# Optimization experiments

Measured on AMD Instinct MI355X. Metric: run time of the kernel, lower is better.

The kernel has to match this reference:

```python
import jax, jax.numpy as jnp
import numpy as np

CANVAS_SIZE = 512
N_POINTS = 64


def setup_inputs() -> dict:
    key = jax.random.key(0)
    k1, _ = jax.random.split(key)
    traj = jax.random.uniform(k1, (N_POINTS, 2), dtype=jnp.float32)  # normalized [0,1] path points
    thickness = jnp.asarray(3.0, dtype=jnp.float32)  # stroke width in pixels
    return {"traj": traj, "thickness": thickness}


def reference(traj, thickness):
    S = CANVAS_SIZE
    a = jnp.arange(S, dtype=traj.dtype)
    # torch: x_coords,y_coords = meshgrid(ij); stack((y_coords,x_coords)) -> coords[i,j] = (j, i)
    row, col = jnp.meshgrid(a, a, indexing="ij")
    p = jnp.stack((col, row), axis=-1)  # (S, S, 2)

    t = traj * S
    v = t[:-1][:, None, None, :]  # (n-1, 1, 1, 2) segment starts
    w = t[1:][:, None, None, :]   # (n-1, 1, 1, 2) segment ends
    seg = w - v                   # (n-1, 1, 1, 2)
    d2 = jnp.sum(seg * seg, axis=-1)  # (n-1, 1, 1) == |v-w|^2
    # projection parameter onto each segment, clamped to [0, 1]
    tt = jnp.clip(jnp.sum((p - v) * seg, axis=-1) / (d2 + 1e-5), 0.0, 1.0)  # (n-1, S, S)
    proj = v + tt[..., None] * seg                      # (n-1, S, S, 2)
    dist = jnp.linalg.norm(p - proj, axis=-1)           # (n-1, S, S)
    dist = jnp.min(dist, axis=0)                        # (S, S) min over segments

    radius = thickness / 2
    darkness = jnp.clip((radius - dist) / radius, 0.0, 1.0)
    return darkness
```

## Files before the change

### kernel.cpp

```cpp
#include <hip/hip_runtime.h>

#define CANVAS 512
#define NPTS 64
#define NSEG (NPTS - 1)

__global__ __launch_bounds__(256) void diff_path_render(
    const float* __restrict__ traj,
    const float* __restrict__ thickness,
    float* __restrict__ out)
{
    const int t = blockIdx.x * blockDim.x + threadIdx.x;
    const int pix0 = t * 2;
    const int row = pix0 >> 9;
    const int col0 = pix0 & (CANVAS - 1);

    const float INV_S = 1.0f / 512.0f;
    const float py  = (float)row  * INV_S;
    const float px0 = (float)col0 * INV_S;
    const float px1 = px0 + INV_S;
    const float EPS = 1e-5f / (512.0f * 512.0f);

    float m0 = 1e30f, m1 = 1e30f;

    float ax = traj[0], ay = traj[1];
#pragma unroll 9
    for (int s = 0; s < NSEG; ++s) {
        float bx = traj[2 * s + 2];
        float by = traj[2 * s + 3];
        float segx = bx - ax, segy = by - ay;
        float d2  = fmaf(segx, segx, fmaf(segy, segy, EPS));
        float inv = __builtin_amdgcn_rcpf(d2);

        float dy  = py  - ay;
        float dx0 = px0 - ax;
        float dx1 = px1 - ax;
        float dysy = dy * segy;

        float t0 = fmaf(dx0, segx, dysy) * inv;
        float t1 = fmaf(dx1, segx, dysy) * inv;
        t0 = fminf(fmaxf(t0, 0.0f), 1.0f);
        t1 = fminf(fmaxf(t1, 0.0f), 1.0f);

        float qx0 = fmaf(-t0, segx, dx0);
        float qy0 = fmaf(-t0, segy, dy);
        float qx1 = fmaf(-t1, segx, dx1);
        float qy1 = fmaf(-t1, segy, dy);

        float dd0 = fmaf(qx0, qx0, qy0 * qy0);
        float dd1 = fmaf(qx1, qx1, qy1 * qy1);
        m0 = fminf(m0, dd0);
        m1 = fminf(m1, dd1);

        ax = bx; ay = by;
    }

    const float radius = thickness[0] * 0.5f;
    const float rinv = __builtin_amdgcn_rcpf(radius);
    const float d0 = 512.0f * sqrtf(m0);
    const float d1 = 512.0f * sqrtf(m1);
    const float o0 = fminf(fmaxf((radius - d0) * rinv, 0.0f), 1.0f);
    const float o1 = fminf(fmaxf((radius - d1) * rinv, 0.0f), 1.0f);

    *reinterpret_cast<float2*>(out + pix0) = make_float2(o0, o1);
}

extern "C" void kernel_launch(void* const* d_in, const int* in_sizes, int n_in,
                              void* d_out, int out_size, void* d_ws, size_t ws_size,
                              hipStream_t stream) {
    const float* traj      = (const float*)d_in[0];
    const float* thickness = (const float*)d_in[1];
    float* out = (float*)d_out;

    const int threads = CANVAS * CANVAS / 2;
    const int block = 256;
    const int grid = threads / block;
    diff_path_render<<<grid, block, 0, stream>>>(traj, thickness, out);
}
```

Baseline: 11.51 us.

## Compute four pixels per thread using packed float2 vector math

Each thread now handles four adjacent pixels instead of two. The per-pixel math is expressed with two-wide vector types so the compiler can emit packed FP32 instructions (v_pk_fma_f32 etc.) on CDNA, and the result is written with one float4 store. This spreads the per-segment setup (loads, reciprocal, dy terms) over more pixels and halves the grid size. In exchange, occupancy and wave count drop and register pressure rises.

Result: faster. 11.17 us, median of 2 (-3.0%).

```diff
diff --git a/kernel.cpp b/kernel.cpp
--- a/kernel.cpp
+++ b/kernel.cpp
@@ -3,6 +3,8 @@
 #define CANVAS 512
 #define NPTS 64
 #define NSEG (NPTS - 1)
+
+typedef float f2 __attribute__((ext_vector_type(2)));
 
 __global__ __launch_bounds__(256) void diff_path_render(
     const float* __restrict__ traj,
@@ -10,17 +12,18 @@
     float* __restrict__ out)
 {
     const int t = blockIdx.x * blockDim.x + threadIdx.x;
-    const int pix0 = t * 2;
-    const int row = pix0 >> 9;
+    const int pix0 = t * 4;
+    const int row  = pix0 >> 9;
     const int col0 = pix0 & (CANVAS - 1);
 
     const float INV_S = 1.0f / 512.0f;
-    const float py  = (float)row  * INV_S;
-    const float px0 = (float)col0 * INV_S;
-    const float px1 = px0 + INV_S;
+    const float py = (float)row * INV_S;
+    const f2 px01 = { (float)(col0 + 0) * INV_S, (float)(col0 + 1) * INV_S };
+    const f2 px23 = { (float)(col0 + 2) * INV_S, (float)(col0 + 3) * INV_S };
     const float EPS = 1e-5f / (512.0f * 512.0f);
 
-    float m0 = 1e30f, m1 = 1e30f;
+    f2 m01 = { 1e30f, 1e30f };
+    f2 m23 = { 1e30f, 1e30f };
 
     float ax = traj[0], ay = traj[1];
 #pragma unroll 9
@@ -31,37 +34,50 @@
         float d2  = fmaf(segx, segx, fmaf(segy, segy, EPS));
         float inv = __builtin_amdgcn_rcpf(d2);
 
-        float dy  = py  - ay;
-        float dx0 = px0 - ax;
-        float dx1 = px1 - ax;
+        float dy   = py - ay;
         float dysy = dy * segy;
 
-        float t0 = fmaf(dx0, segx, dysy) * inv;
-        float t1 = fmaf(dx1, segx, dysy) * inv;
-        t0 = fminf(fmaxf(t0, 0.0f), 1.0f);
-        t1 = fminf(fmaxf(t1, 0.0f), 1.0f);
+        const f2 segxv = { segx, segx };
+        const f2 segyv = { segy, segy };
+        const f2 dysyv = { dysy, dysy };
+        const f2 axv   = { ax, ax };
+        const f2 invv  = { inv, inv };
+        const f2 zero  = { 0.0f, 0.0f };
+        const f2 one   = { 1.0f, 1.0f };
 
-        float qx0 = fmaf(-t0, segx, dx0);
-        float qy0 = fmaf(-t0, segy, dy);
-        float qx1 = fmaf(-t1, segx, dx1);
-        float qy1 = fmaf(-t1, segy, dy);
+        f2 dx01 = px01 - axv;
+        f2 dx23 = px23 - axv;
+        f2 t01 = __builtin_elementwise_fma(dx01, segxv, dysyv);
+        f2 t23 = __builtin_elementwise_fma(dx23, segxv, dysyv);
+        t01 = t01 * invv;
+        t23 = t23 * invv;
+        t01 = __builtin_elementwise_min(__builtin_elementwise_max(t01, zero), one);
+        t23 = __builtin_elementwise_min(__builtin_elementwise_max(t23, zero), one);
 
-        float dd0 = fmaf(qx0, qx0, qy0 * qy0);
-        float dd1 = fmaf(qx1, qx1, qy1 * qy1);
-        m0 = fminf(m0, dd0);
-        m1 = fminf(m1, dd1);
+        f2 qx01 = __builtin_elementwise_fma(-t01, segxv, dx01);
+        f2 qx23 = __builtin_elementwise_fma(-t23, segxv, dx23);
+        f2 dyv  = { dy, dy };
+        f2 qy01 = __builtin_elementwise_fma(-t01, segyv, dyv);
+        f2 qy23 = __builtin_elementwise_fma(-t23, segyv, dyv);
+
+        f2 dd01 = __builtin_elementwise_fma(qx01, qx01, qy01 * qy01);
+        f2 dd23 = __builtin_elementwise_fma(qx23, qx23, qy23 * qy23);
+        m01 = __builtin_elementwise_min(m01, dd01);
+        m23 = __builtin_elementwise_min(m23, dd23);
 
         ax = bx; ay = by;
     }
 
     const float radius = thickness[0] * 0.5f;
     const float rinv = __builtin_amdgcn_rcpf(radius);
-    const float d0 = 512.0f * sqrtf(m0);
-    const float d1 = 512.0f * sqrtf(m1);
-    const float o0 = fminf(fmaxf((radius - d0) * rinv, 0.0f), 1.0f);
-    const float o1 = fminf(fmaxf((radius - d1) * rinv, 0.0f), 1.0f);
 
-    *reinterpret_cast<float2*>(out + pix0) = make_float2(o0, o1);
+    float4 o;
+    o.x = fminf(fmaxf((radius - 512.0f * sqrtf(m01.x)) * rinv, 0.0f), 1.0f);
+    o.y = fminf(fmaxf((radius - 512.0f * sqrtf(m01.y)) * rinv, 0.0f), 1.0f);
+    o.z = fminf(fmaxf((radius - 512.0f * sqrtf(m23.x)) * rinv, 0.0f), 1.0f);
+    o.w = fminf(fmaxf((radius - 512.0f * sqrtf(m23.y)) * rinv, 0.0f), 1.0f);
+
+    *reinterpret_cast<float4*>(out + pix0) = o;
 }
 
 extern "C" void kernel_launch(void* const* d_in, const int* in_sizes, int n_in,
@@ -71,7 +87,7 @@
     const float* thickness = (const float*)d_in[1];
     float* out = (float*)d_out;
 
-    const int threads = CANVAS * CANVAS / 2;
+    const int threads = CANVAS * CANVAS / 4;
     const int block = 256;
     const int grid = threads / block;
     diff_path_render<<<grid, block, 0, stream>>>(traj, thickness, out);
```
